# Kernel tuning notes

Hardware: AMD Instinct MI355X
Metric: run time of the kernel (lower is better)

The kernel has to match this reference:

```python
import jax, jax.numpy as jnp
import numpy as np

STRIDE = 16
A = 9
PRE_NMS_TOP_N = 6000
POST_NMS_TOP_N = 300
NMS_THRESH = 0.7
MIN_SIZE = 16
H, W = 128, 192


def _generate_anchors(base_size=16, ratios=(0.5, 1.0, 2.0), scales=(8, 16, 32)):
    base = np.array([0, 0, base_size - 1, base_size - 1], dtype=np.float64)
    w = base[2] - base[0] + 1
    h = base[3] - base[1] + 1
    x_ctr = base[0] + 0.5 * (w - 1)
    y_ctr = base[1] + 0.5 * (h - 1)
    size = w * h
    ratios = np.array(ratios)
    ws = np.round(np.sqrt(size / ratios))
    hs = np.round(ws * ratios)
    ratio_anchors = np.stack([x_ctr - 0.5 * (ws - 1), y_ctr - 0.5 * (hs - 1),
                              x_ctr + 0.5 * (ws - 1), y_ctr + 0.5 * (hs - 1)], axis=1)
    out = []
    scales = np.array(scales)
    for a in ratio_anchors:
        aw = a[2] - a[0] + 1
        ah = a[3] - a[1] + 1
        xc = a[0] + 0.5 * (aw - 1)
        yc = a[1] + 0.5 * (ah - 1)
        ws2 = aw * scales
        hs2 = ah * scales
        out.append(np.stack([xc - 0.5 * (ws2 - 1), yc - 0.5 * (hs2 - 1),
                             xc + 0.5 * (ws2 - 1), yc + 0.5 * (hs2 - 1)], axis=1))
    return np.concatenate(out, axis=0).astype(np.float32)  # [9,4]


def setup_inputs() -> dict:
    key = jax.random.key(0)
    k1, k2 = jax.random.split(key)
    scores = jax.random.uniform(k1, (1, 2 * A, H, W), dtype=jnp.float32)
    bbox_deltas = 0.1 * jax.random.normal(k2, (1, 4 * A, H, W), dtype=jnp.float32)
    im_info = jnp.array([[H * STRIDE, W * STRIDE, 1.0]], dtype=jnp.float32)
    return {"scores": scores, "bbox_deltas": bbox_deltas, "im_info": im_info}


def _proposal_forward(scores, bbox_deltas, im_info):
    anchors_base = jnp.asarray(_generate_anchors())  # [A,4]
    sc = scores[:, A:, :, :]                          # fg scores [1,A,H,W]
    h, w = sc.shape[-2], sc.shape[-1]
    shift_x = (jnp.arange(w) * STRIDE).astype(sc.dtype)
    shift_y = (jnp.arange(h) * STRIDE).astype(sc.dtype)
    sy, sx = jnp.meshgrid(shift_y, shift_x, indexing='ij')
    shifts = jnp.stack([sx.ravel(), sy.ravel(), sx.ravel(), sy.ravel()], axis=1)  # [K,4]
    anchors = (anchors_base[None, :, :] + shifts[:, None, :]).reshape(-1, 4)      # [K*A,4]

    deltas = bbox_deltas.transpose(0, 2, 3, 1).reshape(-1, 4)
    deltas = jnp.concatenate([deltas[:, :2], jnp.clip(deltas[:, 2:], -10.0, 10.0)], axis=1)
    sc = sc.transpose(0, 2, 3, 1).reshape(-1)  # [K*A]

    widths = anchors[:, 2] - anchors[:, 0] + 1.0
    heights = anchors[:, 3] - anchors[:, 1] + 1.0
    ctr_x = anchors[:, 0] + 0.5 * widths
    ctr_y = anchors[:, 1] + 0.5 * heights
    dx, dy, dw, dh = deltas[:, 0], deltas[:, 1], deltas[:, 2], deltas[:, 3]
    pcx = dx * widths + ctr_x
    pcy = dy * heights + ctr_y
    pw = jnp.exp(dw) * widths
    ph = jnp.exp(dh) * heights
    x1 = pcx - 0.5 * pw
    y1 = pcy - 0.5 * ph
    x2 = pcx + 0.5 * pw
    y2 = pcy + 0.5 * ph

    info = im_info[0]
    x1 = jnp.clip(x1, 0.0, info[1] - 1.0)
    x2 = jnp.clip(x2, 0.0, info[1] - 1.0)
    y1 = jnp.clip(y1, 0.0, info[0] - 1.0)
    y2 = jnp.clip(y2, 0.0, info[0] - 1.0)
    proposals = jnp.stack([x1, y1, x2, y2], axis=1)

    # filter_boxes: mask (instead of dropping) boxes smaller than min_size*scale
    min_sz = MIN_SIZE * info[2]
    valid = ((x2 - x1 + 1.0) >= min_sz) & ((y2 - y1 + 1.0) >= min_sz)
    masked = jnp.where(valid, sc, -jnp.inf)

    # sort desc + pre_nms_topN
    top_scores, top_idx = jax.lax.top_k(masked, PRE_NMS_TOP_N)
    boxes = proposals[top_idx]               # [PRE,4], score-descending
    tvalid = top_scores > -jnp.inf

    # pairwise IoU (torchvision convention)
    area = (boxes[:, 2] - boxes[:, 0]) * (boxes[:, 3] - boxes[:, 1])
    lt = jnp.maximum(boxes[:, None, :2], boxes[None, :, :2])
    rb = jnp.minimum(boxes[:, None, 2:], boxes[None, :, 2:])
    wh = jnp.clip(rb - lt, 0.0)
    inter = wh[..., 0] * wh[..., 1]
    iou = inter / (area[:, None] + area[None, :] - inter)  # [PRE,PRE]

    # greedy NMS over score-sorted boxes
    n = PRE_NMS_TOP_N
    def step(keep, x):
        iou_col, v, i = x
        suppressed = jnp.any(keep & (iou_col > NMS_THRESH))
        k = v & jnp.logical_not(suppressed)
        keep = keep.at[i].set(k)
        return keep, k
    keep, _ = jax.lax.scan(step, jnp.zeros((n,), dtype=bool),
                           (iou.T, tvalid, jnp.arange(n)))

    # kept boxes first (stable => score order preserved), take post_nms_topN
    order = jnp.argsort(jnp.logical_not(keep).astype(jnp.int32), stable=True)[:POST_NMS_TOP_N]
    kept = keep[order]
    out_boxes = jnp.where(kept[:, None], boxes[order], 0.0)
    output = jnp.concatenate(
        [jnp.zeros((POST_NMS_TOP_N, 1), out_boxes.dtype), out_boxes], axis=1)
    return output  # [POST,5]: (batch_idx=0, x1,y1,x2,y2); rows beyond kept count are zero


def reference(scores, bbox_deltas, im_info):
    return _proposal_forward(scores, bbox_deltas, im_info)
```

## Files before the change

### kernel.cpp

```cpp
#include <hip/hip_runtime.h>

#define N_ANCH 221184
#define HW     24576
#define Wd     192
#define AA     9
#define TOPN   6000
#define POSTN  300
#define CAND_CAP 8192
#define NWORDS 94
#define NCHUNK 47

typedef unsigned long long u64;

__device__ const float c_aw[9] = {184.f,368.f,736.f,128.f,256.f,512.f, 88.f,176.f,352.f};
__device__ const float c_ah[9] = { 96.f,192.f,384.f,128.f,256.f,512.f,176.f,352.f,704.f};

__device__ __forceinline__ float4 decode_box(int a, int cell,
                                             const float* __restrict__ deltas,
                                             float info0, float info1, float info2,
                                             bool* valid) {
    int h = cell / Wd;
    int w = cell - h * Wd;
    const float* db = deltas + (size_t)(4 * a) * HW + cell;
    float dx = db[0];
    float dy = db[HW];
    float dw = db[2 * HW];
    float dh = db[3 * HW];
    dw = fminf(fmaxf(dw, -10.f), 10.f);
    dh = fminf(fmaxf(dh, -10.f), 10.f);

    float ww = c_aw[a], hh = c_ah[a];
    float cx = 16.f * (float)w + 8.f;
    float cy = 16.f * (float)h + 8.f;

    float pcx = __fadd_rn(__fmul_rn(dx, ww), cx);
    float pcy = __fadd_rn(__fmul_rn(dy, hh), cy);
    float pw  = __fmul_rn(expf(dw), ww);
    float ph  = __fmul_rn(expf(dh), hh);
    float hpw = __fmul_rn(0.5f, pw);
    float hph = __fmul_rn(0.5f, ph);
    float x1 = __fsub_rn(pcx, hpw);
    float x2 = __fadd_rn(pcx, hpw);
    float y1 = __fsub_rn(pcy, hph);
    float y2 = __fadd_rn(pcy, hph);

    float xmax = __fsub_rn(info1, 1.f);
    float ymax = __fsub_rn(info0, 1.f);
    x1 = fminf(fmaxf(x1, 0.f), xmax);
    x2 = fminf(fmaxf(x2, 0.f), xmax);
    y1 = fminf(fmaxf(y1, 0.f), ymax);
    y2 = fminf(fmaxf(y2, 0.f), ymax);

    float msz = __fmul_rn(16.f, info2);
    *valid = (__fadd_rn(__fsub_rn(x2, x1), 1.f) >= msz) &&
             (__fadd_rn(__fsub_rn(y2, y1), 1.f) >= msz);
    return make_float4(x1, y1, x2, y2);
}

#define ZA_F4 4164
#define ZB_F4 48
__global__ __launch_bounds__(256) void init_kernel(float4* zA, float4* zB) {
    int t = blockIdx.x * 256 + threadIdx.x;
    float4 z = make_float4(0.f, 0.f, 0.f, 0.f);
    if (t < ZA_F4) zA[t] = z;
    else if (t < ZA_F4 + ZB_F4) zB[t - ZA_F4] = z;
}

__global__ __launch_bounds__(256) void decode_kernel(const float* __restrict__ scores,
                                                     const float* __restrict__ deltas,
                                                     const float* __restrict__ iminfo,
                                                     unsigned int* __restrict__ keys,
                                                     unsigned int* __restrict__ hist256) {
    __shared__ unsigned int lh[256];
    lh[threadIdx.x] = 0u;
    __syncthreads();
    int t = blockIdx.x * 256 + threadIdx.x;
    int a = t / HW;
    int cell = t - a * HW;
    float score = scores[(AA + a) * HW + cell];
    bool valid;
    (void)decode_box(a, cell, deltas, iminfo[0], iminfo[1], iminfo[2], &valid);
    unsigned int sb = __float_as_uint(score);
    unsigned int key = valid ? ((sb & 0x80000000u) ? ~sb : (sb | 0x80000000u))
                             : 0x007FFFFFu;
    keys[t] = key;
    atomicAdd(&lh[key >> 24], 1u);
    __syncthreads();
    if (lh[threadIdx.x]) atomicAdd(&hist256[threadIdx.x], lh[threadIdx.x]);
}

__global__ __launch_bounds__(1024) void midselect_kernel(const unsigned int* __restrict__ keys,
                                                         const unsigned int* __restrict__ hist256,
                                                         unsigned int* __restrict__ state) {
    __shared__ unsigned int sfx[256];
    __shared__ unsigned int h2w[16][256];
    __shared__ unsigned int sP, sRank;
    int t = threadIdx.x;
    int wv = t >> 6;
    for (int i = t; i < 16 * 256; i += 1024) ((unsigned int*)h2w)[i] = 0u;
    if (t < 256) sfx[t] = hist256[t];
    __syncthreads();
    for (int d = 1; d < 256; d <<= 1) {
        unsigned int v = 0u;
        if (t < 256 && t + d < 256) v = sfx[t + d];
        __syncthreads();
        if (t < 256) sfx[t] += v;
        __syncthreads();
    }
    if (t < 256) {
        unsigned int ge = sfx[t];
        unsigned int gt = (t < 255) ? sfx[t + 1] : 0u;
        if (ge >= TOPN && gt < TOPN) { sP = (unsigned int)t; sRank = TOPN - gt; }
    }
    __syncthreads();
    unsigned int P = sP, rank = sRank;
    const uint4* k4 = (const uint4*)keys;
    for (int i = t; i < N_ANCH / 4; i += 1024) {
        uint4 v = k4[i];
        if ((v.x >> 24) == P) atomicAdd(&h2w[wv][(v.x >> 16) & 0xFFu], 1u);
        if ((v.y >> 24) == P) atomicAdd(&h2w[wv][(v.y >> 16) & 0xFFu], 1u);
        if ((v.z >> 24) == P) atomicAdd(&h2w[wv][(v.z >> 16) & 0xFFu], 1u);
        if ((v.w >> 24) == P) atomicAdd(&h2w[wv][(v.w >> 16) & 0xFFu], 1u);
    }
    __syncthreads();
    if (t < 256) {
        unsigned int s = 0;
        #pragma unroll
        for (int wvi = 0; wvi < 16; ++wvi) s += h2w[wvi][t];
        sfx[t] = s;
    }
    __syncthreads();
    for (int d = 1; d < 256; d <<= 1) {
        unsigned int v = 0u;
        if (t < 256 && t + d < 256) v = sfx[t + d];
        __syncthreads();
        if (t < 256) sfx[t] += v;
        __syncthreads();
    }
    if (t < 256) {
        unsigned int ge = sfx[t];
        unsigned int gt = (t < 255) ? sfx[t + 1] : 0u;
        if (ge >= rank && gt < rank) {
            state[0] = (P << 24) | ((unsigned int)t << 16);
            state[2] = 0u;
        }
    }
}

__global__ __launch_bounds__(256) void compact_kernel(const unsigned int* __restrict__ keys,
                                                      unsigned int* __restrict__ state,
                                                      u64* __restrict__ cand) {
    int t = blockIdx.x * 256 + threadIdx.x;
    unsigned int k = keys[t];
    unsigned int T = state[0];
    if (k >= T) {
        unsigned int pos = atomicAdd(&state[2], 1u);
        if (pos < CAND_CAP) {
            int a = t / HW;
            int cell = t - a * HW;
            unsigned int aidx = (unsigned int)(cell * 9 + a);
            cand[pos] = ((u64)k << 32) | (u64)(~aidx);
        }
    }
}

__global__ __launch_bounds__(256) void rank_scatter_kernel(const u64* __restrict__ cand,
                                                           const float* __restrict__ deltas,
                                                           const float* __restrict__ iminfo,
                                                           float4* __restrict__ tb,
                                                           u64* __restrict__ vmask) {
    __shared__ u64 s[CAND_CAP];
    for (int j = threadIdx.x; j < CAND_CAP; j += 256) s[j] = cand[j];
    int part = threadIdx.x & 7;
    int i = blockIdx.x * 32 + (threadIdx.x >> 3);
    u64 k = cand[i];
    __syncthreads();
    const ulonglong2* sv = (const ulonglong2*)s;
    unsigned int cnt = 0;
    #pragma unroll 8
    for (int jj = part; jj < CAND_CAP / 2; jj += 8) {
        ulonglong2 v = sv[jj];
        cnt += (v.x > k) ? 1u : 0u;
        cnt += (v.y > k) ? 1u : 0u;
    }
    cnt += __shfl_xor(cnt, 1);
    cnt += __shfl_xor(cnt, 2);
    cnt += __shfl_xor(cnt, 4);
    if (part == 0 && k != 0ull && cnt < TOPN) {
        unsigned int aidx = ~((unsigned int)k);
        int a = (int)(aidx % 9u);
        int cell = (int)(aidx / 9u);
        bool valid;
        float4 box = decode_box(a, cell, deltas, iminfo[0], iminfo[1], iminfo[2], &valid);
        tb[cnt] = box;
        if ((unsigned int)(k >> 32) != 0x007FFFFFu)
            atomicOr(&vmask[cnt >> 6], 1ull << (cnt & 63));
    }
}

__global__ __launch_bounds__(64) void nms_matrix_kernel(const float4* __restrict__ tb,
                                                        u64* __restrict__ mat) {
    if (blockIdx.x < blockIdx.y) return;
    __shared__ float4 cb[64];
    int t = threadIdx.x;
    int c0 = blockIdx.x * 64;
    int col = c0 + t;
    cb[t] = (col < TOPN) ? tb[col] : make_float4(0.f, 0.f, 0.f, 0.f);
    __syncthreads();
    int row = blockIdx.y * 64 + t;
    if (row >= TOPN) return;
    float4 rb = tb[row];
    float rA = (rb.z - rb.x) * (rb.w - rb.y);
    u64 mask = 0ull;
    for (int c = 0; c < 64; ++c) {
        if (c0 + c >= TOPN) break;
        float4 b = cb[c];
        float lx = fmaxf(rb.x, b.x), ly = fmaxf(rb.y, b.y);
        float rx = fminf(rb.z, b.z), ry = fminf(rb.w, b.w);
        float iw = fmaxf(rx - lx, 0.f), ih = fmaxf(ry - ly, 0.f);
        float inter = iw * ih;
        float bA = (b.z - b.x) * (b.w - b.y);
        float iou = inter / ((rA + bA) - inter);
        if (iou > 0.7f) mask |= (1ull << c);
    }
    mat[(size_t)row * NWORDS + blockIdx.x] = mask;
}

__device__ __forceinline__ u64 rdl64(u64 v, int l) {
    unsigned int lo = (unsigned int)__builtin_amdgcn_readlane((int)(unsigned int)v, l);
    unsigned int hi = (unsigned int)__builtin_amdgcn_readlane((int)(unsigned int)(v >> 32), l);
    return ((u64)hi << 32) | (u64)lo;
}

__global__ __launch_bounds__(64) void nms_scan_kernel(const u64* __restrict__ mat,
                                                      const u64* __restrict__ vmask,
                                                      const float4* __restrict__ tb,
                                                      float* __restrict__ out) {
    int lane = threadIdx.x;
    u64 r0 = ~vmask[lane];
    u64 r1 = (lane < NWORDS - 64) ? ~vmask[64 + lane] : ~0ull;
    __shared__ int kept[POSTN];
    int cnt = 0;

    u64 a0, a1, b0, b1;
    {
        ulonglong2 vA = *(const ulonglong2*)(mat + (size_t)lane * NWORDS);
        ulonglong2 vB = *(const ulonglong2*)(mat + (size_t)(64 + lane) * NWORDS);
        a0 = vA.x; a1 = vA.y; b0 = vB.x; b1 = vB.y;
    }
    for (int c = 0; c < NCHUNK; ++c) {
        u64 na0 = 0, na1 = 0, nb0 = 0, nb1 = 0;
        if (c + 1 < NCHUNK) {
            const u64* pA = mat + (size_t)((c + 1) * 128 + lane) * NWORDS + 2 * (c + 1);
            const u64* pB = mat + (size_t)((c + 1) * 128 + 64 + lane) * NWORDS + 2 * (c + 1);
            ulonglong2 vA = *(const ulonglong2*)pA;
            ulonglong2 vB = *(const ulonglong2*)pB;
            na0 = vA.x; na1 = vA.y; nb0 = vB.x; nb1 = vB.y;
        }
        int w2 = 2 * c;
        u64 s0 = (w2 < 64) ? rdl64(r0, w2) : rdl64(r1, w2 - 64);
        u64 s1 = (w2 + 1 < 64) ? rdl64(r0, w2 + 1) : rdl64(r1, w2 + 1 - 64);
        if ((s0 & s1) != ~0ull) {
            int base = c * 128;
            u64 rem0 = s0, rem1 = s1, k0 = 0ull, k1 = 0ull;
            while (cnt < POSTN) {
                int b;
                if (~rem0) b = __ffsll((u64)~rem0) - 1;
                else if (~rem1) b = 64 + __ffsll((u64)~rem1) - 1;
                else break;
                if (lane == 0) kept[cnt] = base + b;
                ++cnt;
                u64 w0, w1;
                if (b < 64) {
                    w0 = rdl64(a0, b); w1 = rdl64(a1, b);
                    k0 |= 1ull << b; rem0 |= 1ull << b;
                } else {
                    int bb = b - 64;
                    w0 = rdl64(b0, bb); w1 = rdl64(b1, bb);
                    k1 |= 1ull << bb; rem1 |= 1ull << bb;
                }
                rem0 |= w0; rem1 |= w1;
            }
            if (cnt >= POSTN) break;
            u64 f0 = 0ull, f1 = 0ull, m0 = k0, m1 = k1;
            while (m0 | m1) {
                int idxs[8];
                #pragma unroll
                for (int j = 0; j < 8; ++j) {
                    int b = -1;
                    if (m0) { b = __ffsll(m0) - 1; m0 &= m0 - 1; }
                    else if (m1) { b = 64 + __ffsll(m1) - 1; m1 &= m1 - 1; }
                    idxs[j] = b;
                }
                u64 v0[8], v1[8];
                #pragma unroll
                for (int j = 0; j < 8; ++j) {
                    v0[j] = 0ull; v1[j] = 0ull;
                    if (idxs[j] >= 0) {
                        const u64* row = mat + (size_t)(base + idxs[j]) * NWORDS;
                        v0[j] = row[lane];
                        if (lane < NWORDS - 64) v1[j] = row[64 + lane];
                    }
                }
                #pragma unroll
                for (int j = 0; j < 8; ++j) { f0 |= v0[j]; f1 |= v1[j]; }
            }
            r0 |= f0; r1 |= f1;
        }
        a0 = na0; a1 = na1; b0 = nb0; b1 = nb1;
    }

    for (int r = lane; r < POSTN; r += 64) {
        float4 b = make_float4(0.f, 0.f, 0.f, 0.f);
        if (r < cnt) b = tb[kept[r]];
        float* o = out + r * 5;
        o[0] = 0.f; o[1] = b.x; o[2] = b.y; o[3] = b.z; o[4] = b.w;
    }
}

extern "C" void kernel_launch(void* const* d_in, const int* in_sizes, int n_in,
                              void* d_out, int out_size, void* d_ws, size_t ws_size,
                              hipStream_t stream) {
    const float* scores = (const float*)d_in[0];
    const float* deltas = (const float*)d_in[1];
    const float* iminfo = (const float*)d_in[2];
    float* out = (float*)d_out;

    char* ws = (char*)d_ws;
    unsigned int* keys    = (unsigned int*)(ws + 0);
    unsigned int* hist256 = (unsigned int*)(ws + 884736);
    unsigned int* state   = (unsigned int*)(ws + 885760);
    u64*          cand    = (u64*)(ws + 885824);
    float4*       tb      = (float4*)(ws + 951360);
    u64*          vmask   = (u64*)(ws + 1047616);
    u64*          mat     = (u64*)(ws + 1048384);

    const int NB = N_ANCH / 256;

    init_kernel<<<17, 256, 0, stream>>>((float4*)hist256, (float4*)vmask);
    decode_kernel<<<NB, 256, 0, stream>>>(scores, deltas, iminfo, keys, hist256);
    midselect_kernel<<<1, 1024, 0, stream>>>(keys, hist256, state);
    compact_kernel<<<NB, 256, 0, stream>>>(keys, state, cand);
    rank_scatter_kernel<<<CAND_CAP / 32, 256, 0, stream>>>(cand, deltas, iminfo, tb, vmask);
    nms_matrix_kernel<<<dim3(NWORDS, NWORDS), 64, 0, stream>>>(tb, mat);
    nms_scan_kernel<<<1, 64, 0, stream>>>(mat, vmask, tb, out);
}
```

Baseline: 249.0 us.

## Fuse proposal pipeline into one cooperative persistent kernel with grid syncs

Replaces the seven separate launches with one cooperative kernel of 512 blocks that moves through decode/histogram, threshold select, compaction, rank-scatter, IoU matrix and greedy scan, separated by grid-wide barriers. If the cooperative launch fails it falls back to launching each phase separately. Per-block histogram slabs replace global atomics, the second histogram pass is spread across the grid instead of one block, and compaction goes to eight segmented counters. The goal is to remove launch gaps and the single-block serial selection pass, at the cost of grid-sync overhead, a serial 512-slab reduction in one block, and dropping the prefetch of the next chunk in the scan.

```diff
diff --git a/kernel.cpp b/kernel.cpp
--- a/kernel.cpp
+++ b/kernel.cpp
@@ -1,4 +1,7 @@
 #include <hip/hip_runtime.h>
+#include <hip/hip_cooperative_groups.h>
+
+namespace cg = cooperative_groups;
 
 #define N_ANCH 221184
 #define HW     24576
@@ -6,9 +9,11 @@
 #define AA     9
 #define TOPN   6000
 #define POSTN  300
-#define CAND_CAP 8192
 #define NWORDS 94
 #define NCHUNK 47
+#define GRID   512
+#define STRIDE0 (GRID * 256)
+#define SEGSZ  1024
 
 typedef unsigned long long u64;
 
@@ -57,211 +62,228 @@
     return make_float4(x1, y1, x2, y2);
 }
 
-#define ZA_F4 4164
-#define ZB_F4 48
-__global__ __launch_bounds__(256) void init_kernel(float4* zA, float4* zB) {
-    int t = blockIdx.x * 256 + threadIdx.x;
-    float4 z = make_float4(0.f, 0.f, 0.f, 0.f);
-    if (t < ZA_F4) zA[t] = z;
-    else if (t < ZA_F4 + ZB_F4) zB[t - ZA_F4] = z;
-}
-
-__global__ __launch_bounds__(256) void decode_kernel(const float* __restrict__ scores,
-                                                     const float* __restrict__ deltas,
-                                                     const float* __restrict__ iminfo,
-                                                     unsigned int* __restrict__ keys,
-                                                     unsigned int* __restrict__ hist256) {
-    __shared__ unsigned int lh[256];
-    lh[threadIdx.x] = 0u;
-    __syncthreads();
-    int t = blockIdx.x * 256 + threadIdx.x;
-    int a = t / HW;
-    int cell = t - a * HW;
-    float score = scores[(AA + a) * HW + cell];
-    bool valid;
-    (void)decode_box(a, cell, deltas, iminfo[0], iminfo[1], iminfo[2], &valid);
-    unsigned int sb = __float_as_uint(score);
-    unsigned int key = valid ? ((sb & 0x80000000u) ? ~sb : (sb | 0x80000000u))
-                             : 0x007FFFFFu;
-    keys[t] = key;
-    atomicAdd(&lh[key >> 24], 1u);
-    __syncthreads();
-    if (lh[threadIdx.x]) atomicAdd(&hist256[threadIdx.x], lh[threadIdx.x]);
-}
-
-__global__ __launch_bounds__(1024) void midselect_kernel(const unsigned int* __restrict__ keys,
-                                                         const unsigned int* __restrict__ hist256,
-                                                         unsigned int* __restrict__ state) {
-    __shared__ unsigned int sfx[256];
-    __shared__ unsigned int h2w[16][256];
-    __shared__ unsigned int sP, sRank;
-    int t = threadIdx.x;
-    int wv = t >> 6;
-    for (int i = t; i < 16 * 256; i += 1024) ((unsigned int*)h2w)[i] = 0u;
-    if (t < 256) sfx[t] = hist256[t];
-    __syncthreads();
-    for (int d = 1; d < 256; d <<= 1) {
-        unsigned int v = 0u;
-        if (t < 256 && t + d < 256) v = sfx[t + d];
-        __syncthreads();
-        if (t < 256) sfx[t] += v;
-        __syncthreads();
-    }
-    if (t < 256) {
-        unsigned int ge = sfx[t];
-        unsigned int gt = (t < 255) ? sfx[t + 1] : 0u;
-        if (ge >= TOPN && gt < TOPN) { sP = (unsigned int)t; sRank = TOPN - gt; }
-    }
-    __syncthreads();
-    unsigned int P = sP, rank = sRank;
-    const uint4* k4 = (const uint4*)keys;
-    for (int i = t; i < N_ANCH / 4; i += 1024) {
-        uint4 v = k4[i];
-        if ((v.x >> 24) == P) atomicAdd(&h2w[wv][(v.x >> 16) & 0xFFu], 1u);
-        if ((v.y >> 24) == P) atomicAdd(&h2w[wv][(v.y >> 16) & 0xFFu], 1u);
-        if ((v.z >> 24) == P) atomicAdd(&h2w[wv][(v.z >> 16) & 0xFFu], 1u);
-        if ((v.w >> 24) == P) atomicAdd(&h2w[wv][(v.w >> 16) & 0xFFu], 1u);
-    }
-    __syncthreads();
-    if (t < 256) {
-        unsigned int s = 0;
-        #pragma unroll
-        for (int wvi = 0; wvi < 16; ++wvi) s += h2w[wvi][t];
-        sfx[t] = s;
-    }
-    __syncthreads();
-    for (int d = 1; d < 256; d <<= 1) {
-        unsigned int v = 0u;
-        if (t < 256 && t + d < 256) v = sfx[t + d];
-        __syncthreads();
-        if (t < 256) sfx[t] += v;
-        __syncthreads();
-    }
-    if (t < 256) {
-        unsigned int ge = sfx[t];
-        unsigned int gt = (t < 255) ? sfx[t + 1] : 0u;
-        if (ge >= rank && gt < rank) {
-            state[0] = (P << 24) | ((unsigned int)t << 16);
-            state[2] = 0u;
-        }
-    }
-}
-
-__global__ __launch_bounds__(256) void compact_kernel(const unsigned int* __restrict__ keys,
-                                                      unsigned int* __restrict__ state,
-                                                      u64* __restrict__ cand) {
-    int t = blockIdx.x * 256 + threadIdx.x;
-    unsigned int k = keys[t];
-    unsigned int T = state[0];
-    if (k >= T) {
-        unsigned int pos = atomicAdd(&state[2], 1u);
-        if (pos < CAND_CAP) {
-            int a = t / HW;
-            int cell = t - a * HW;
-            unsigned int aidx = (unsigned int)(cell * 9 + a);
-            cand[pos] = ((u64)k << 32) | (u64)(~aidx);
-        }
-    }
-}
-
-__global__ __launch_bounds__(256) void rank_scatter_kernel(const u64* __restrict__ cand,
-                                                           const float* __restrict__ deltas,
-                                                           const float* __restrict__ iminfo,
-                                                           float4* __restrict__ tb,
-                                                           u64* __restrict__ vmask) {
-    __shared__ u64 s[CAND_CAP];
-    for (int j = threadIdx.x; j < CAND_CAP; j += 256) s[j] = cand[j];
-    int part = threadIdx.x & 7;
-    int i = blockIdx.x * 32 + (threadIdx.x >> 3);
-    u64 k = cand[i];
-    __syncthreads();
-    const ulonglong2* sv = (const ulonglong2*)s;
-    unsigned int cnt = 0;
-    #pragma unroll 8
-    for (int jj = part; jj < CAND_CAP / 2; jj += 8) {
-        ulonglong2 v = sv[jj];
-        cnt += (v.x > k) ? 1u : 0u;
-        cnt += (v.y > k) ? 1u : 0u;
-    }
-    cnt += __shfl_xor(cnt, 1);
-    cnt += __shfl_xor(cnt, 2);
-    cnt += __shfl_xor(cnt, 4);
-    if (part == 0 && k != 0ull && cnt < TOPN) {
-        unsigned int aidx = ~((unsigned int)k);
-        int a = (int)(aidx % 9u);
-        int cell = (int)(aidx / 9u);
-        bool valid;
-        float4 box = decode_box(a, cell, deltas, iminfo[0], iminfo[1], iminfo[2], &valid);
-        tb[cnt] = box;
-        if ((unsigned int)(k >> 32) != 0x007FFFFFu)
-            atomicOr(&vmask[cnt >> 6], 1ull << (cnt & 63));
-    }
-}
-
-__global__ __launch_bounds__(64) void nms_matrix_kernel(const float4* __restrict__ tb,
-                                                        u64* __restrict__ mat) {
-    if (blockIdx.x < blockIdx.y) return;
-    __shared__ float4 cb[64];
-    int t = threadIdx.x;
-    int c0 = blockIdx.x * 64;
-    int col = c0 + t;
-    cb[t] = (col < TOPN) ? tb[col] : make_float4(0.f, 0.f, 0.f, 0.f);
-    __syncthreads();
-    int row = blockIdx.y * 64 + t;
-    if (row >= TOPN) return;
-    float4 rb = tb[row];
-    float rA = (rb.z - rb.x) * (rb.w - rb.y);
-    u64 mask = 0ull;
-    for (int c = 0; c < 64; ++c) {
-        if (c0 + c >= TOPN) break;
-        float4 b = cb[c];
-        float lx = fmaxf(rb.x, b.x), ly = fmaxf(rb.y, b.y);
-        float rx = fminf(rb.z, b.z), ry = fminf(rb.w, b.w);
-        float iw = fmaxf(rx - lx, 0.f), ih = fmaxf(ry - ly, 0.f);
-        float inter = iw * ih;
-        float bA = (b.z - b.x) * (b.w - b.y);
-        float iou = inter / ((rA + bA) - inter);
-        if (iou > 0.7f) mask |= (1ull << c);
-    }
-    mat[(size_t)row * NWORDS + blockIdx.x] = mask;
-}
-
 __device__ __forceinline__ u64 rdl64(u64 v, int l) {
     unsigned int lo = (unsigned int)__builtin_amdgcn_readlane((int)(unsigned int)v, l);
     unsigned int hi = (unsigned int)__builtin_amdgcn_readlane((int)(unsigned int)(v >> 32), l);
     return ((u64)hi << 32) | (u64)lo;
 }
 
-__global__ __launch_bounds__(64) void nms_scan_kernel(const u64* __restrict__ mat,
-                                                      const u64* __restrict__ vmask,
-                                                      const float4* __restrict__ tb,
-                                                      float* __restrict__ out) {
-    int lane = threadIdx.x;
-    u64 r0 = ~vmask[lane];
-    u64 r1 = (lane < NWORDS - 64) ? ~vmask[64 + lane] : ~0ull;
+__global__ __launch_bounds__(256, 2) void fused_kernel(
+        const float* __restrict__ scores, const float* __restrict__ deltas,
+        const float* __restrict__ iminfo, float* __restrict__ out,
+        unsigned int* __restrict__ keys, unsigned int* __restrict__ slab,
+        unsigned int* __restrict__ slab2, unsigned int* __restrict__ state,
+        u64* __restrict__ cand, float4* __restrict__ tb,
+        u64* __restrict__ vmask, u64* __restrict__ mat, int phase) {
+    const bool all = (phase < 0);
+    int tid = threadIdx.x;
+    int bid = blockIdx.x;
+    int lane = tid & 63;
+    int wv = tid >> 6;
+
+    __shared__ unsigned int lh[256];
+    __shared__ unsigned int sfx[256];
+    __shared__ unsigned int h2w[4][256];
+    __shared__ u64 stage[2048];
+    __shared__ float4 cbw[4][64];
     __shared__ int kept[POSTN];
-    int cnt = 0;
-
-    u64 a0, a1, b0, b1;
-    {
-        ulonglong2 vA = *(const ulonglong2*)(mat + (size_t)lane * NWORDS);
-        ulonglong2 vB = *(const ulonglong2*)(mat + (size_t)(64 + lane) * NWORDS);
-        a0 = vA.x; a1 = vA.y; b0 = vB.x; b1 = vB.y;
-    }
-    for (int c = 0; c < NCHUNK; ++c) {
-        u64 na0 = 0, na1 = 0, nb0 = 0, nb1 = 0;
-        if (c + 1 < NCHUNK) {
-            const u64* pA = mat + (size_t)((c + 1) * 128 + lane) * NWORDS + 2 * (c + 1);
-            const u64* pB = mat + (size_t)((c + 1) * 128 + 64 + lane) * NWORDS + 2 * (c + 1);
-            ulonglong2 vA = *(const ulonglong2*)pA;
-            ulonglong2 vB = *(const ulonglong2*)pB;
-            na0 = vA.x; na1 = vA.y; nb0 = vB.x; nb1 = vB.y;
-        }
-        int w2 = 2 * c;
-        u64 s0 = (w2 < 64) ? rdl64(r0, w2) : rdl64(r1, w2 - 64);
-        u64 s1 = (w2 + 1 < 64) ? rdl64(r0, w2 + 1) : rdl64(r1, w2 + 1 - 64);
-        if ((s0 & s1) != ~0ull) {
+
+    float info0 = iminfo[0], info1 = iminfo[1], info2 = iminfo[2];
+
+    if (all || phase == 0) {
+        lh[tid] = 0u;
+        __syncthreads();
+        #pragma unroll
+        for (int j = 0; j < 2; ++j) {
+            int t = j * STRIDE0 + bid * 256 + tid;
+            if (t < N_ANCH) {
+                int a = t / HW;
+                int cell = t - a * HW;
+                float score = scores[(AA + a) * HW + cell];
+                bool valid;
+                (void)decode_box(a, cell, deltas, info0, info1, info2, &valid);
+                unsigned int sb = __float_as_uint(score);
+                unsigned int key = valid ? ((sb & 0x80000000u) ? ~sb : (sb | 0x80000000u))
+                                         : 0x007FFFFFu;
+                keys[t] = key;
+                atomicAdd(&lh[key >> 24], 1u);
+            }
+        }
+        __syncthreads();
+        slab[bid * 256 + tid] = lh[tid];
+    }
+    if (all) { __threadfence(); cg::this_grid().sync(); }
+
+    if ((all && bid == 0) || phase == 1) {
+        state[tid] = 0u;
+        state[256 + tid] = 0u;
+        if (tid < 96) vmask[tid] = 0ull;
+        unsigned int s = 0;
+        for (int b = 0; b < GRID; ++b) s += slab[b * 256 + tid];
+        sfx[tid] = s;
+        __syncthreads();
+        for (int d = 1; d < 256; d <<= 1) {
+            unsigned int v = (tid + d < 256) ? sfx[tid + d] : 0u;
+            __syncthreads();
+            sfx[tid] += v;
+            __syncthreads();
+        }
+        unsigned int ge = sfx[tid];
+        unsigned int gt = (tid < 255) ? sfx[tid + 1] : 0u;
+        if (ge >= TOPN && gt < TOPN) { state[1] = (unsigned int)tid; state[2] = TOPN - gt; }
+    }
+    if (all) { __threadfence(); cg::this_grid().sync(); }
+
+    if (all || phase == 2) {
+        for (int i = tid; i < 4 * 256; i += 256) ((unsigned int*)h2w)[i] = 0u;
+        __syncthreads();
+        unsigned int P = *(volatile unsigned int*)&state[1];
+        #pragma unroll
+        for (int j = 0; j < 2; ++j) {
+            int t = j * STRIDE0 + bid * 256 + tid;
+            if (t < N_ANCH) {
+                unsigned int k = keys[t];
+                if ((k >> 24) == P) atomicAdd(&h2w[wv][(k >> 16) & 0xFFu], 1u);
+            }
+        }
+        __syncthreads();
+        slab2[bid * 256 + tid] = h2w[0][tid] + h2w[1][tid] + h2w[2][tid] + h2w[3][tid];
+    }
+    if (all) { __threadfence(); cg::this_grid().sync(); }
+
+    if ((all && bid == 0) || phase == 3) {
+        unsigned int P = *(volatile unsigned int*)&state[1];
+        unsigned int rankP = *(volatile unsigned int*)&state[2];
+        unsigned int s = 0;
+        for (int b = 0; b < GRID; ++b) s += slab2[b * 256 + tid];
+        sfx[tid] = s;
+        __syncthreads();
+        for (int d = 1; d < 256; d <<= 1) {
+            unsigned int v = (tid + d < 256) ? sfx[tid + d] : 0u;
+            __syncthreads();
+            sfx[tid] += v;
+            __syncthreads();
+        }
+        unsigned int ge = sfx[tid];
+        unsigned int gt = (tid < 255) ? sfx[tid + 1] : 0u;
+        if (ge >= rankP && gt < rankP)
+            state[0] = (P << 24) | ((unsigned int)tid << 16);
+    }
+    if (all) { __threadfence(); cg::this_grid().sync(); }
+
+    if (all || phase == 4) {
+        unsigned int T = *(volatile unsigned int*)&state[0];
+        #pragma unroll
+        for (int j = 0; j < 2; ++j) {
+            int t = j * STRIDE0 + bid * 256 + tid;
+            if (t < N_ANCH) {
+                unsigned int k = keys[t];
+                if (k >= T) {
+                    int seg = bid & 7;
+                    unsigned int pos = atomicAdd(&state[32 + 32 * seg], 1u);
+                    if (pos < SEGSZ) {
+                        int a = t / HW;
+                        int cell = t - a * HW;
+                        unsigned int aidx = (unsigned int)(cell * 9 + a);
+                        cand[seg * SEGSZ + pos] = ((u64)k << 32) | (u64)(~aidx);
+                    }
+                }
+            }
+        }
+    }
+    if (all) { __threadfence(); cg::this_grid().sync(); }
+
+    if (all || phase == 5) {
+        unsigned int cc[8];
+        #pragma unroll
+        for (int s = 0; s < 8; ++s) {
+            cc[s] = *(volatile unsigned int*)&state[32 + 32 * s];
+            if (cc[s] > SEGSZ) cc[s] = SEGSZ;
+        }
+        int part = tid & 15;
+        int i = bid * 16 + (tid >> 4);
+        int iseg = i >> 10, ioff = i & 1023;
+        bool active = (unsigned int)ioff < cc[iseg];
+        u64 k = active ? cand[i] : 0ull;
+        unsigned int cnt = 0;
+        for (int q = 0; q < 4; ++q) {
+            for (int j = tid; j < 2048; j += 256) {
+                int g = q * 2048 + j;
+                int s_ = g >> 10, off = g & 1023;
+                stage[j] = ((unsigned int)off < cc[s_]) ? cand[g] : 0ull;
+            }
+            __syncthreads();
+            const ulonglong2* sv = (const ulonglong2*)stage;
+            for (int jj = part; jj < 1024; jj += 16) {
+                ulonglong2 v = sv[jj];
+                cnt += (v.x > k) ? 1u : 0u;
+                cnt += (v.y > k) ? 1u : 0u;
+            }
+            __syncthreads();
+        }
+        cnt += __shfl_xor(cnt, 1);
+        cnt += __shfl_xor(cnt, 2);
+        cnt += __shfl_xor(cnt, 4);
+        cnt += __shfl_xor(cnt, 8);
+        if (part == 0 && active && cnt < TOPN) {
+            unsigned int aidx = ~((unsigned int)k);
+            int a = (int)(aidx % 9u);
+            int cell = (int)(aidx / 9u);
+            bool valid;
+            float4 box = decode_box(a, cell, deltas, info0, info1, info2, &valid);
+            tb[cnt] = box;
+            if ((unsigned int)(k >> 32) != 0x007FFFFFu)
+                atomicOr(&vmask[cnt >> 6], 1ull << (cnt & 63));
+        }
+    }
+    if (all) { __threadfence(); cg::this_grid().sync(); }
+
+    if (all || phase == 6) {
+        int waveid = bid * 4 + wv;
+        int wstride = gridDim.x * 4;
+        for (int j = waveid; j < 94 * 94; j += wstride) {
+            int by = j / 94;
+            int bx = j - by * 94;
+            if (bx < by) continue;
+            int c0 = bx * 64;
+            {
+                int col = c0 + lane;
+                cbw[wv][lane] = (col < TOPN) ? tb[col] : make_float4(0.f, 0.f, 0.f, 0.f);
+            }
+            int row = by * 64 + lane;
+            if (row < TOPN) {
+                float4 rb = tb[row];
+                float rA = (rb.z - rb.x) * (rb.w - rb.y);
+                u64 mask = 0ull;
+                for (int c = 0; c < 64; ++c) {
+                    if (c0 + c >= TOPN) break;
+                    float4 b = cbw[wv][c];
+                    float lx = fmaxf(rb.x, b.x), ly = fmaxf(rb.y, b.y);
+                    float rx = fminf(rb.z, b.z), ry = fminf(rb.w, b.w);
+                    float iw = fmaxf(rx - lx, 0.f), ih = fmaxf(ry - ly, 0.f);
+                    float inter = iw * ih;
+                    float bA = (b.z - b.x) * (b.w - b.y);
+                    float iou = inter / ((rA + bA) - inter);
+                    if (iou > 0.7f) mask |= (1ull << c);
+                }
+                mat[(size_t)row * NWORDS + bx] = mask;
+            }
+        }
+    }
+    if (all) { __threadfence(); cg::this_grid().sync(); }
+
+    if (((all && bid == 0) || phase == 7) && tid < 64) {
+        u64 r0 = ~vmask[lane];
+        u64 r1 = (lane < NWORDS - 64) ? ~vmask[64 + lane] : ~0ull;
+        int cnt = 0;
+        for (int c = 0; c < NCHUNK; ++c) {
+            int w2 = 2 * c;
+            u64 s0 = (w2 < 64) ? rdl64(r0, w2) : rdl64(r1, w2 - 64);
+            u64 s1 = (w2 + 1 < 64) ? rdl64(r0, w2 + 1) : rdl64(r1, w2 + 1 - 64);
+            if ((s0 & s1) == ~0ull) continue;
             int base = c * 128;
+            ulonglong2 vA = *(const ulonglong2*)(mat + (size_t)(base + lane) * NWORDS + w2);
+            ulonglong2 vB = *(const ulonglong2*)(mat + (size_t)(base + 64 + lane) * NWORDS + w2);
             u64 rem0 = s0, rem1 = s1, k0 = 0ull, k1 = 0ull;
             while (cnt < POSTN) {
                 int b;
@@ -270,51 +292,49 @@
                 else break;
                 if (lane == 0) kept[cnt] = base + b;
                 ++cnt;
-                u64 w0, w1;
                 if (b < 64) {
-                    w0 = rdl64(a0, b); w1 = rdl64(a1, b);
-                    k0 |= 1ull << b; rem0 |= 1ull << b;
+                    rem0 |= rdl64(vA.x, b) | (1ull << b);
+                    rem1 |= rdl64(vA.y, b);
+                    k0 |= 1ull << b;
                 } else {
                     int bb = b - 64;
-                    w0 = rdl64(b0, bb); w1 = rdl64(b1, bb);
-                    k1 |= 1ull << bb; rem1 |= 1ull << bb;
-                }
-                rem0 |= w0; rem1 |= w1;
+                    rem0 |= rdl64(vB.x, bb);
+                    rem1 |= rdl64(vB.y, bb) | (1ull << bb);
+                    k1 |= 1ull << bb;
+                }
             }
             if (cnt >= POSTN) break;
             u64 f0 = 0ull, f1 = 0ull, m0 = k0, m1 = k1;
             while (m0 | m1) {
-                int idxs[8];
+                int idx[16];
                 #pragma unroll
-                for (int j = 0; j < 8; ++j) {
+                for (int j = 0; j < 16; ++j) {
                     int b = -1;
                     if (m0) { b = __ffsll(m0) - 1; m0 &= m0 - 1; }
                     else if (m1) { b = 64 + __ffsll(m1) - 1; m1 &= m1 - 1; }
-                    idxs[j] = b;
-                }
-                u64 v0[8], v1[8];
+                    idx[j] = b;
+                }
+                u64 v0[16], v1[16];
                 #pragma unroll
-                for (int j = 0; j < 8; ++j) {
+                for (int j = 0; j < 16; ++j) {
                     v0[j] = 0ull; v1[j] = 0ull;
-                    if (idxs[j] >= 0) {
-                        const u64* row = mat + (size_t)(base + idxs[j]) * NWORDS;
+                    if (idx[j] >= 0) {
+                        const u64* row = mat + (size_t)(base + idx[j]) * NWORDS;
                         v0[j] = row[lane];
                         if (lane < NWORDS - 64) v1[j] = row[64 + lane];
                     }
                 }
                 #pragma unroll
-                for (int j = 0; j < 8; ++j) { f0 |= v0[j]; f1 |= v1[j]; }
+                for (int j = 0; j < 16; ++j) { f0 |= v0[j]; f1 |= v1[j]; }
             }
             r0 |= f0; r1 |= f1;
         }
-        a0 = na0; a1 = na1; b0 = nb0; b1 = nb1;
-    }
-
-    for (int r = lane; r < POSTN; r += 64) {
-        float4 b = make_float4(0.f, 0.f, 0.f, 0.f);
-        if (r < cnt) b = tb[kept[r]];
-        float* o = out + r * 5;
-        o[0] = 0.f; o[1] = b.x; o[2] = b.y; o[3] = b.z; o[4] = b.w;
+        for (int r = lane; r < POSTN; r += 64) {
+            float4 b2 = make_float4(0.f, 0.f, 0.f, 0.f);
+            if (r < cnt) b2 = tb[kept[r]];
+            float* o = out + r * 5;
+            o[0] = 0.f; o[1] = b2.x; o[2] = b2.y; o[3] = b2.z; o[4] = b2.w;
+        }
     }
 }
 
@@ -327,21 +347,39 @@
     float* out = (float*)d_out;
 
     char* ws = (char*)d_ws;
-    unsigned int* keys    = (unsigned int*)(ws + 0);
-    unsigned int* hist256 = (unsigned int*)(ws + 884736);
-    unsigned int* state   = (unsigned int*)(ws + 885760);
-    u64*          cand    = (u64*)(ws + 885824);
-    float4*       tb      = (float4*)(ws + 951360);
-    u64*          vmask   = (u64*)(ws + 1047616);
-    u64*          mat     = (u64*)(ws + 1048384);
-
-    const int NB = N_ANCH / 256;
-
-    init_kernel<<<17, 256, 0, stream>>>((float4*)hist256, (float4*)vmask);
-    decode_kernel<<<NB, 256, 0, stream>>>(scores, deltas, iminfo, keys, hist256);
-    midselect_kernel<<<1, 1024, 0, stream>>>(keys, hist256, state);
-    compact_kernel<<<NB, 256, 0, stream>>>(keys, state, cand);
-    rank_scatter_kernel<<<CAND_CAP / 32, 256, 0, stream>>>(cand, deltas, iminfo, tb, vmask);
-    nms_matrix_kernel<<<dim3(NWORDS, NWORDS), 64, 0, stream>>>(tb, mat);
-    nms_scan_kernel<<<1, 64, 0, stream>>>(mat, vmask, tb, out);
+    unsigned int* keys  = (unsigned int*)(ws + 0);
+    unsigned int* slab  = (unsigned int*)(ws + 884736);
+    unsigned int* slab2 = (unsigned int*)(ws + 1409024);
+    unsigned int* state = (unsigned int*)(ws + 1933312);
+    u64*          cand  = (u64*)(ws + 1935360);
+    float4*       tb    = (float4*)(ws + 2000896);
+    u64*          vmask = (u64*)(ws + 2097152);
+    u64*          mat   = (u64*)(ws + 2097920);
+
+    int phase_all = -1;
+    void* args[] = { (void*)&scores, (void*)&deltas, (void*)&iminfo, (void*)&out,
+                     (void*)&keys, (void*)&slab, (void*)&slab2, (void*)&state,
+                     (void*)&cand, (void*)&tb, (void*)&vmask, (void*)&mat,
+                     (void*)&phase_all };
+    hipError_t err = hipLaunchCooperativeKernel((void*)fused_kernel, dim3(GRID),
+                                                dim3(256), args, 0, stream);
+    if (err != hipSuccess) {
+        (void)hipGetLastError();
+        fused_kernel<<<GRID, 256, 0, stream>>>(scores, deltas, iminfo, out, keys, slab,
+                                               slab2, state, cand, tb, vmask, mat, 0);
+        fused_kernel<<<1,    256, 0, stream>>>(scores, deltas, iminfo, out, keys, slab,
+                                               slab2, state, cand, tb, vmask, mat, 1);
+        fused_kernel<<<GRID, 256, 0, stream>>>(scores, deltas, iminfo, out, keys, slab,
+                                               slab2, state, cand, tb, vmask, mat, 2);
+        fused_kernel<<<1,    256, 0, stream>>>(scores, deltas, iminfo, out, keys, slab,
+                                               slab2, state, cand, tb, vmask, mat, 3);
+        fused_kernel<<<GRID, 256, 0, stream>>>(scores, deltas, iminfo, out, keys, slab,
+                                               slab2, state, cand, tb, vmask, mat, 4);
+        fused_kernel<<<GRID, 256, 0, stream>>>(scores, deltas, iminfo, out, keys, slab,
+                                               slab2, state, cand, tb, vmask, mat, 5);
+        fused_kernel<<<GRID, 256, 0, stream>>>(scores, deltas, iminfo, out, keys, slab,
+                                               slab2, state, cand, tb, vmask, mat, 6);
+        fused_kernel<<<1,    256, 0, stream>>>(scores, deltas, iminfo, out, keys, slab,
+                                               slab2, state, cand, tb, vmask, mat, 7);
+    }
 }
```

New measurement: 864.1 us. 247% more time.
